# Optimization experiments

Measured on AMD Instinct MI355X. Metric: run time of the kernel, lower is better.

The kernel has to match this reference:

```python
import jax, jax.numpy as jnp
import numpy as np

IMG_SIZE = 256
NUM_ANGLES = 180
NUM_DETECTORS = 363  # ceil(sqrt(2)*256)


def setup_inputs() -> dict:
    key = jax.random.key(0)
    x = jax.random.normal(key, (4, 1, IMG_SIZE, IMG_SIZE), dtype=jnp.float32)
    return {"x": x}


def _radon(x):
    # x: (B,1,H,W) -> sinogram (B,1,A,D). Faithful to RadonTransform.forward
    # (grid_sample rotate, sum rows, bilinear resize detector axis, align_corners=True).
    B, C, H, W = x.shape
    A, D = NUM_ANGLES, NUM_DETECTORS
    angles = jnp.linspace(0.0, np.pi * (1.0 - 1.0 / A), A, dtype=x.dtype)
    yc = jnp.linspace(-1.0, 1.0, H, dtype=x.dtype)
    xc = jnp.linspace(-1.0, 1.0, W, dtype=x.dtype)
    yy, xx = jnp.meshgrid(yc, xc, indexing='ij')          # (H,W)
    cos_t = jnp.cos(-angles)[:, None, None]               # (A,1,1)
    sin_t = jnp.sin(-angles)[:, None, None]
    gx = xx[None] * cos_t - yy[None] * sin_t              # (A,H,W) normalized x coord
    gy = xx[None] * sin_t + yy[None] * cos_t              # (A,H,W) normalized y coord
    # grid_sample bilinear, padding_mode='zeros', align_corners=True
    fx = (gx + 1.0) * 0.5 * (W - 1)
    fy = (gy + 1.0) * 0.5 * (H - 1)
    x0 = jnp.floor(fx).astype(jnp.int32); x1 = x0 + 1
    y0 = jnp.floor(fy).astype(jnp.int32); y1 = y0 + 1
    wx = fx - x0.astype(x.dtype)
    wy = fy - y0.astype(x.dtype)
    img = x[:, 0]                                         # (B,H,W)

    def tap(yi, xi):
        valid = (yi >= 0) & (yi < H) & (xi >= 0) & (xi < W)
        ycl = jnp.clip(yi, 0, H - 1)
        xcl = jnp.clip(xi, 0, W - 1)
        v = img[:, ycl, xcl]                              # (B,A,H,W)
        return jnp.where(valid[None], v, jnp.zeros((), x.dtype))

    sampled = (tap(y0, x0) * ((1 - wy) * (1 - wx))[None]
               + tap(y0, x1) * ((1 - wy) * wx)[None]
               + tap(y1, x0) * (wy * (1 - wx))[None]
               + tap(y1, x1) * (wy * wx)[None])           # (B,A,H,W)
    proj = sampled.sum(axis=2)                            # (B,A,W) sum along rows (dim=2)
    # F.interpolate to (A, D), bilinear, align_corners=True; angle axis is identity.
    pos = jnp.arange(D, dtype=x.dtype) * (W - 1) / (D - 1)
    p0 = jnp.floor(pos).astype(jnp.int32)
    p1 = jnp.minimum(p0 + 1, W - 1)
    w = pos - p0.astype(x.dtype)
    sino = proj[:, :, p0] * (1.0 - w) + proj[:, :, p1] * w  # (B,A,D)
    return sino[:, None]                                   # (B,1,A,D)


def reference(x):
    # CTForwardModel.forward(x, add_noise=False): noiseless sinogram = Radon(x)
    return _radon(x)
```

## Files before the change

### kernel.cpp

```cpp
#include <hip/hip_runtime.h>
#include <hip/hip_fp16.h>
#include <math.h>

#define IMG   256
#define NANG  180
#define NDET  363
#define PAD   3
#define PS    264
#define PSZ   (PS * PS)
#define TEX_BYTES ((size_t)2 * PSZ * 8)
#define PP_BYTES  ((size_t)NANG * 4 * IMG * 16)
#define WS_NEED   (TEX_BYTES + PP_BYTES)

__device__ __forceinline__ __half2 u2h2(unsigned u) {
    return *reinterpret_cast<__half2*>(&u);
}
__device__ __forceinline__ unsigned h22u(__half2 h) {
    return *reinterpret_cast<unsigned*>(&h);
}

__global__ __launch_bounds__(1024) void prep_kernel(const float* __restrict__ x,
                                                    uint2* __restrict__ ws) {
    __shared__ uint2 tile[32][33];
    const int tx = threadIdx.x, ty = threadIdx.y;
    const int px = blockIdx.x * 32 + tx;
    const int py = blockIdx.y * 32 + ty;
    const int ix = px - PAD, iy = py - PAD;

    uint2 t = make_uint2(0u, 0u);
    if ((unsigned)ix < IMG && (unsigned)iy < IMG) {
        const size_t o = (size_t)iy * IMG + ix;
        const __half2 lo = __floats2half2_rn(x[o],                 x[o + IMG * IMG]);
        const __half2 hi = __floats2half2_rn(x[o + 2 * IMG * IMG], x[o + 3 * IMG * IMG]);
        t.x = h22u(lo);
        t.y = h22u(hi);
    }
    if (px < PS && py < PS) ws[(size_t)py * PS + px] = t;
    tile[ty][tx] = t;
    __syncthreads();
    const int opx = blockIdx.y * 32 + tx;
    const int opy = blockIdx.x * 32 + ty;
    if (opx < PS && opy < PS)
        ws[(size_t)PSZ + (size_t)opy * PS + opx] = tile[tx][ty];
}

__global__ __launch_bounds__(512) void radon_main(const uint2* __restrict__ ws,
                                                  float4* __restrict__ proj_part) {
    const int a  = blockIdx.x;
    const int q  = blockIdx.y;
    const int j  = threadIdx.x & 255;
    const int iq = threadIdx.x >> 8;

    const float ang = (float)a * 0.017453292519943295f;
    const float cs = cosf(ang);
    const float sn = -sinf(ang);

    const float xcj = -1.0f + (2.0f / 255.0f) * (float)j;
    const float fx0 = 127.5f * (xcj * cs + sn + 1.0f);
    const float dfx = -sn;
    const float fy0 = 127.5f * (xcj * sn - cs + 1.0f);
    const float dfy = cs;

    const bool swp = fabsf(sn) > fabsf(cs);
    const float rc0 = swp ? fx0 : fy0;  const float drow = swp ? dfx : dfy;
    const float cc0 = swp ? fy0 : fx0;  const float dcol = swp ? dfy : dfx;
    const uint2* __restrict__ base = ws + (swp ? PSZ : 0);

    float lo = 0.0f, hi = 255.0f;
    if (fabsf(drow) > 1e-5f) {
        const float t1 = (-1.5f - rc0) / drow, t2 = (256.5f - rc0) / drow;
        lo = fmaxf(lo, fminf(t1, t2));
        hi = fminf(hi, fmaxf(t1, t2));
    } else if (rc0 < -1.5f || rc0 > 256.5f) { lo = 1.0f; hi = 0.0f; }
    if (fabsf(dcol) > 1e-5f) {
        const float t1 = (-1.5f - cc0) / dcol, t2 = (256.5f - cc0) / dcol;
        lo = fmaxf(lo, fminf(t1, t2));
        hi = fminf(hi, fmaxf(t1, t2));
    } else if (cc0 < -1.5f || cc0 > 256.5f) { lo = 1.0f; hi = 0.0f; }

    const int tlo = q * 64 + iq * 32;
    const int ilo = max(max(0,   (int)floorf(lo)), tlo);
    const int ihi = min(min(255, (int)ceilf(hi)), tlo + 31);

    float4 sum = make_float4(0.f, 0.f, 0.f, 0.f);
    #pragma unroll 4
    for (int i = ilo; i <= ihi; ++i) {
        const float rc = fmaf((float)i, drow, rc0);
        const float cc = fmaf((float)i, dcol, cc0);
        const float rf = floorf(rc);
        const float cf = floorf(cc);
        const float wr = rc - rf;
        const float wc = cc - cf;
        const int idx = (int)fmaf(rf, (float)PS, cf) + (PAD * PS + PAD);

        const uint4 tr = *reinterpret_cast<const uint4*>(base + idx);
        const uint4 br = *reinterpret_cast<const uint4*>(base + idx + PS);

        const __half2 wc2 = __float2half2_rn(wc);
        const __half2 wr2 = __float2half2_rn(wr);

        const __half2 v00a = u2h2(tr.x), v00b = u2h2(tr.y);
        const __half2 v01a = u2h2(tr.z), v01b = u2h2(tr.w);
        const __half2 v10a = u2h2(br.x), v10b = u2h2(br.y);
        const __half2 v11a = u2h2(br.z), v11b = u2h2(br.w);

        const __half2 topa = __hfma2(wc2, __hsub2(v01a, v00a), v00a);
        const __half2 topb = __hfma2(wc2, __hsub2(v01b, v00b), v00b);
        const __half2 bota = __hfma2(wc2, __hsub2(v11a, v10a), v10a);
        const __half2 botb = __hfma2(wc2, __hsub2(v11b, v10b), v10b);
        const __half2 ra = __hfma2(wr2, __hsub2(bota, topa), topa);
        const __half2 rb = __hfma2(wr2, __hsub2(botb, topb), topb);

        sum.x += __low2float(ra);
        sum.y += __high2float(ra);
        sum.z += __low2float(rb);
        sum.w += __high2float(rb);
    }

    __shared__ float4 part[2][IMG];
    part[iq][j] = sum;
    __syncthreads();
    if (iq == 0) {
        const float4 o = part[1][j];
        float4 s = part[0][j];
        s.x += o.x; s.y += o.y; s.z += o.z; s.w += o.w;
        proj_part[(size_t)(a * 4 + q) * IMG + j] = s;
    }
}

__global__ __launch_bounds__(384) void detect_kernel(const float4* __restrict__ proj_part,
                                                     float* __restrict__ out) {
    const int a = blockIdx.x;
    const int t = threadIdx.x;
    __shared__ float4 proj[IMG];
    if (t < IMG) {
        float4 s = proj_part[(size_t)(a * 4 + 0) * IMG + t];
        #pragma unroll
        for (int qq = 1; qq < 4; ++qq) {
            const float4 p = proj_part[(size_t)(a * 4 + qq) * IMG + t];
            s.x += p.x; s.y += p.y; s.z += p.z; s.w += p.w;
        }
        proj[t] = s;
    }
    __syncthreads();
    if (t < NDET) {
        const float pos = (float)t * (255.0f / 362.0f);
        const float fp = floorf(pos);
        const int p0 = (int)fp;
        const int p1 = min(p0 + 1, IMG - 1);
        const float w = pos - fp;
        const float4 lo = proj[p0], hi = proj[p1];
        const size_t o = (size_t)a * NDET + t;
        out[o]                   = fmaf(w, hi.x - lo.x, lo.x);
        out[o + 1 * NANG * NDET] = fmaf(w, hi.y - lo.y, lo.y);
        out[o + 2 * NANG * NDET] = fmaf(w, hi.z - lo.z, lo.z);
        out[o + 3 * NANG * NDET] = fmaf(w, hi.w - lo.w, lo.w);
    }
}

__global__ __launch_bounds__(256) void radon_fallback(const float* __restrict__ x,
                                                      float* __restrict__ out) {
    const int blk = blockIdx.x;
    const int a = blk >> 2;
    const int b = blk & 3;
    const int j = threadIdx.x;
    const float* __restrict__ img = x + (size_t)b * (IMG * IMG);
    const float ang = (float)a * 0.017453292519943295f;
    const float cs = cosf(ang);
    const float sn = -sinf(ang);
    const float xcj = -1.0f + (2.0f / 255.0f) * (float)j;
    const float gx0 = xcj * cs;
    const float gy0 = xcj * sn;
    float sum = 0.0f;
    for (int i = 0; i < IMG; ++i) {
        const float yci = -1.0f + (2.0f / 255.0f) * (float)i;
        const float fx = (gx0 - yci * sn + 1.0f) * 127.5f;
        const float fy = (gy0 + yci * cs + 1.0f) * 127.5f;
        const float flx = floorf(fx), fly = floorf(fy);
        const int x0 = (int)flx, y0 = (int)fly;
        const float wx = fx - flx, wy = fy - fly;
        const bool vx0 = ((unsigned)x0 < IMG), vx1 = ((unsigned)(x0 + 1) < IMG);
        const bool vy0 = ((unsigned)y0 < IMG), vy1 = ((unsigned)(y0 + 1) < IMG);
        if (!((vx0 | vx1) & (vy0 | vy1))) continue;
        const int xc0 = min(max(x0, 0), IMG - 1), xc1 = min(max(x0 + 1, 0), IMG - 1);
        const int yc0 = min(max(y0, 0), IMG - 1), yc1 = min(max(y0 + 1, 0), IMG - 1);
        const float* r0 = img + yc0 * IMG;
        const float* r1 = img + yc1 * IMG;
        const float v00 = (vy0 && vx0) ? r0[xc0] : 0.0f;
        const float v01 = (vy0 && vx1) ? r0[xc1] : 0.0f;
        const float v10 = (vy1 && vx0) ? r1[xc0] : 0.0f;
        const float v11 = (vy1 && vx1) ? r1[xc1] : 0.0f;
        sum += (1.0f - wy) * ((1.0f - wx) * v00 + wx * v01)
             +         wy  * ((1.0f - wx) * v10 + wx * v11);
    }
    __shared__ float proj[IMG];
    proj[j] = sum;
    __syncthreads();
    for (int d = j; d < NDET; d += 256) {
        const float pos = (float)d * (255.0f / 362.0f);
        const float fp = floorf(pos);
        const int p0 = (int)fp;
        const int p1 = min(p0 + 1, IMG - 1);
        const float w = pos - fp;
        out[(size_t)b * (NANG * NDET) + a * NDET + d] = proj[p0] * (1.0f - w) + proj[p1] * w;
    }
}

extern "C" void kernel_launch(void* const* d_in, const int* in_sizes, int n_in,
                              void* d_out, int out_size, void* d_ws, size_t ws_size,
                              hipStream_t stream) {
    const float* x = (const float*)d_in[0];
    float* out = (float*)d_out;
    (void)in_sizes; (void)n_in; (void)out_size;

    if (ws_size >= WS_NEED) {
        uint2* tex = (uint2*)d_ws;
        float4* proj_part = (float4*)((char*)d_ws + TEX_BYTES);
        prep_kernel<<<dim3(9, 9), dim3(32, 32), 0, stream>>>(x, tex);
        radon_main<<<dim3(NANG, 4), dim3(512), 0, stream>>>(tex, proj_part);
        detect_kernel<<<dim3(NANG), dim3(384), 0, stream>>>(proj_part, out);
    } else {
        radon_fallback<<<dim3(NANG * 4), dim3(256), 0, stream>>>(x, out);
    }
}
```

Before: 32.98 us.

## Tile radon_main as 16 columns by 4 interleaved rows per wavefront with shuffle reduction

Each block now covers 128 rows and 128 columns. Within a wavefront, 16 adjacent columns are each split across 4 lanes that take interleaved rows, and the lane partial sums are combined with shuffle-xor instead of a shared-memory reduction and barrier. The intent is to make each wavefront's texture gathers cover a compact 2D footprint for better cache locality, and to halve the partial-sum buffer traffic read by detect_kernel. The launch grid presumably has to change to match the new blockIdx.y meaning, and that host-side change is in the part of the code not shown.

After: 31.42 us. 1.05x faster.

```diff
diff --git a/kernel.cpp b/kernel.cpp
--- a/kernel.cpp
+++ b/kernel.cpp
@@ -9,7 +9,7 @@
 #define PS    264
 #define PSZ   (PS * PS)
 #define TEX_BYTES ((size_t)2 * PSZ * 8)
-#define PP_BYTES  ((size_t)NANG * 4 * IMG * 16)
+#define PP_BYTES  ((size_t)NANG * 2 * IMG * 16)
 #define WS_NEED   (TEX_BYTES + PP_BYTES)
 
 __device__ __forceinline__ __half2 u2h2(unsigned u) {
@@ -46,10 +46,14 @@
 
 __global__ __launch_bounds__(512) void radon_main(const uint2* __restrict__ ws,
                                                   float4* __restrict__ proj_part) {
-    const int a  = blockIdx.x;
-    const int q  = blockIdx.y;
-    const int j  = threadIdx.x & 255;
-    const int iq = threadIdx.x >> 8;
+    const int a    = blockIdx.x;
+    const int ih   = blockIdx.y >> 1;
+    const int jh   = blockIdx.y & 1;
+    const int lane = threadIdx.x & 63;
+    const int wv   = threadIdx.x >> 6;
+    const int jj   = lane & 15;
+    const int ii4  = lane >> 4;
+    const int j    = jh * 128 + wv * 16 + jj;
 
     const float ang = (float)a * 0.017453292519943295f;
     const float cs = cosf(ang);
@@ -78,13 +82,19 @@
         hi = fminf(hi, fmaxf(t1, t2));
     } else if (cc0 < -1.5f || cc0 > 256.5f) { lo = 1.0f; hi = 0.0f; }
 
-    const int tlo = q * 64 + iq * 32;
-    const int ilo = max(max(0,   (int)floorf(lo)), tlo);
-    const int ihi = min(min(255, (int)ceilf(hi)), tlo + 31);
+    const int ibase = ih * 128;
+    int ilo_t = max((int)floorf(lo), ibase);
+    int ihi_t = min((int)ceilf(hi), ibase + 127);
+    ihi_t = min(ihi_t, 255);
+    const int d0 = ilo_t - ibase - ii4;
+    const int d1 = ihi_t - ibase - ii4;
+    const int klo = max(0, (d0 + 3) >> 2);
+    const int khi = min(31, d1 >> 2);
 
     float4 sum = make_float4(0.f, 0.f, 0.f, 0.f);
     #pragma unroll 4
-    for (int i = ilo; i <= ihi; ++i) {
+    for (int k = klo; k <= khi; ++k) {
+        const int i = ibase + ii4 + (k << 2);
         const float rc = fmaf((float)i, drow, rc0);
         const float cc = fmaf((float)i, dcol, cc0);
         const float rf = floorf(rc);
@@ -117,14 +127,17 @@
         sum.w += __high2float(rb);
     }
 
-    __shared__ float4 part[2][IMG];
-    part[iq][j] = sum;
-    __syncthreads();
-    if (iq == 0) {
-        const float4 o = part[1][j];
-        float4 s = part[0][j];
-        s.x += o.x; s.y += o.y; s.z += o.z; s.w += o.w;
-        proj_part[(size_t)(a * 4 + q) * IMG + j] = s;
+    sum.x += __shfl_xor(sum.x, 16, 64);
+    sum.y += __shfl_xor(sum.y, 16, 64);
+    sum.z += __shfl_xor(sum.z, 16, 64);
+    sum.w += __shfl_xor(sum.w, 16, 64);
+    sum.x += __shfl_xor(sum.x, 32, 64);
+    sum.y += __shfl_xor(sum.y, 32, 64);
+    sum.z += __shfl_xor(sum.z, 32, 64);
+    sum.w += __shfl_xor(sum.w, 32, 64);
+
+    if (ii4 == 0) {
+        proj_part[(size_t)(a * 2 + ih) * IMG + j] = sum;
     }
 }
 
@@ -134,13 +147,9 @@
     const int t = threadIdx.x;
     __shared__ float4 proj[IMG];
     if (t < IMG) {
-        float4 s = proj_part[(size_t)(a * 4 + 0) * IMG + t];
-        #pragma unroll
-        for (int qq = 1; qq < 4; ++qq) {
-            const float4 p = proj_part[(size_t)(a * 4 + qq) * IMG + t];
-            s.x += p.x; s.y += p.y; s.z += p.z; s.w += p.w;
-        }
-        proj[t] = s;
+        const float4 p0 = proj_part[(size_t)(a * 2 + 0) * IMG + t];
+        const float4 p1 = proj_part[(size_t)(a * 2 + 1) * IMG + t];
+        proj[t] = make_float4(p0.x + p1.x, p0.y + p1.y, p0.z + p1.z, p0.w + p1.w);
     }
     __syncthreads();
     if (t < NDET) {
```
